# Optimization experiments

Measured on AMD Instinct MI355X. Metric: run time of the kernel, lower is better.

## Reference

```python
import jax, jax.numpy as jnp
import numpy as np

K_DIM = 1024
V_DIM = 1024
N_HEADS = 16
LN_EPS = 1e-5


def setup_inputs() -> dict:
    key = jax.random.key(0)
    ks = jax.random.split(key, 5)
    B, S = 16, 4096
    K = jax.random.normal(ks[0], (B, S, K_DIM), jnp.float32)
    V = jax.random.normal(ks[1], (B, S, V_DIM), jnp.float32)
    q = jax.random.normal(ks[2], (K_DIM,), jnp.float32)  # learned query
    w0_w = jax.random.normal(ks[3], (V_DIM, V_DIM), jnp.float32) / np.sqrt(V_DIM)
    w0_b = jnp.zeros((V_DIM,), jnp.float32)
    ln_g = jnp.ones((V_DIM,), jnp.float32)
    ln_b = jnp.zeros((V_DIM,), jnp.float32)
    return {"K": K, "V": V, "q": q, "w0_w": w0_w, "w0_b": w0_b, "ln_g": ln_g, "ln_b": ln_b}


def reference(K, V, q, w0_w, w0_b, ln_g, ln_b):
    B, S, C = K.shape
    H = N_HEADS
    d = C // H
    dv = V.shape[-1] // H
    # norm_query=True
    Q = q / jnp.linalg.norm(q)
    # expand to [B,1,C] then faithful contiguous view -> [B*H,1,d]
    Qh = jnp.broadcast_to(Q, (B, 1, C)).reshape(B * H, 1, d)
    # NOTE: the original uses a plain .view (row-major reshape), NOT a
    # transpose-based head split; we reproduce it exactly.
    Kh = K.reshape(B * H, S, d)
    Vh = V.reshape(B * H, S, dv)
    # torchtext ScaledDotProduct: softmax(Q K^T / sqrt(d)) V
    scale = 1.0 / jnp.sqrt(jnp.asarray(d, K.dtype))
    scores = jnp.einsum("bqd,bkd->bqk", Qh * scale, Kh)  # [B*H,1,S]
    attn = jax.nn.softmax(scores, axis=-1)
    A = jnp.einsum("bqk,bkd->bqd", attn, Vh)  # [B*H,1,dv]
    A = A.reshape(B, 1, H * dv)  # multihead_unshape
    # w0 linear
    A = A @ w0_w.T + w0_b
    # LayerNorm over last dim
    mu = jnp.mean(A, axis=-1, keepdims=True)
    var = jnp.var(A, axis=-1, keepdims=True)
    return ln_g * (A - mu) / jnp.sqrt(var + LN_EPS) + ln_b
```

## Files before the change

### kernel.cpp

```cpp
#include <hip/hip_runtime.h>

#define S_LEN 4096
#define D_HEAD 64
#define NH 16
#define C_DIM 1024
#define B_SZ 16
#define NG 256
#define ATTN_THREADS 512
#define NROWG (ATTN_THREADS / 16)

__global__ __launch_bounds__(ATTN_THREADS) void attn_kernel(
    const float* __restrict__ K, const float* __restrict__ V,
    const float* __restrict__ q, float* __restrict__ A)
{
    const int g   = blockIdx.x;
    const int h   = g & (NH - 1);
    const int tid = threadIdx.x;
    const int sub = tid & 15;
    const int rg  = tid >> 4;

    __shared__ float sc[S_LEN];
    __shared__ float part[NROWG * D_HEAD];
    __shared__ float red[ATTN_THREADS / 64];
    __shared__ float s_scalar;
    __shared__ __align__(16) float s_qs[D_HEAD];

    float p;
    {
        float a0 = q[tid];
        float a1 = q[tid + ATTN_THREADS];
        p = a0 * a0 + a1 * a1;
    }
    #pragma unroll
    for (int off = 32; off; off >>= 1) p += __shfl_xor(p, off);
    if ((tid & 63) == 0) red[tid >> 6] = p;
    __syncthreads();
    if (tid == 0) {
        float t = 0.f;
        #pragma unroll
        for (int w = 0; w < ATTN_THREADS / 64; w++) t += red[w];
        s_scalar = rsqrtf(t) * 0.125f;
    }
    __syncthreads();
    if (tid < D_HEAD) s_qs[tid] = q[h * D_HEAD + tid] * s_scalar;
    __syncthreads();

    const float4 qv = ((const float4*)s_qs)[sub];
    const float* __restrict__ Kg = K + (size_t)g * (S_LEN * D_HEAD);
    const float* __restrict__ Vg = V + (size_t)g * (S_LEN * D_HEAD);

    #pragma unroll 4
    for (int r = rg; r < S_LEN; r += NROWG) {
        float4 kv = ((const float4*)(Kg + r * D_HEAD))[sub];
        float d = kv.x * qv.x + kv.y * qv.y + kv.z * qv.z + kv.w * qv.w;
        d += __shfl_xor(d, 1);
        d += __shfl_xor(d, 2);
        d += __shfl_xor(d, 4);
        d += __shfl_xor(d, 8);
        if (sub == 0) sc[r] = d;
    }
    __syncthreads();

    float m = -3.4e38f;
    for (int i = tid; i < S_LEN; i += ATTN_THREADS) m = fmaxf(m, sc[i]);
    #pragma unroll
    for (int off = 32; off; off >>= 1) m = fmaxf(m, __shfl_xor(m, off));
    if ((tid & 63) == 0) red[tid >> 6] = m;
    __syncthreads();
    m = red[0];
    #pragma unroll
    for (int w = 1; w < ATTN_THREADS / 64; w++) m = fmaxf(m, red[w]);
    __syncthreads();

    float sum = 0.f;
    for (int i = tid; i < S_LEN; i += ATTN_THREADS) {
        float e = __expf(sc[i] - m);
        sc[i] = e;
        sum += e;
    }
    #pragma unroll
    for (int off = 32; off; off >>= 1) sum += __shfl_xor(sum, off);
    if ((tid & 63) == 0) red[tid >> 6] = sum;
    __syncthreads();
    float denom = 0.f;
    #pragma unroll
    for (int w = 0; w < ATTN_THREADS / 64; w++) denom += red[w];
    const float inv_denom = 1.0f / denom;

    float4 acc = make_float4(0.f, 0.f, 0.f, 0.f);
    #pragma unroll 4
    for (int r = rg; r < S_LEN; r += NROWG) {
        float4 vv = ((const float4*)(Vg + r * D_HEAD))[sub];
        float pr = sc[r];
        acc.x += pr * vv.x;
        acc.y += pr * vv.y;
        acc.z += pr * vv.z;
        acc.w += pr * vv.w;
    }
    ((float4*)part)[rg * 16 + sub] = acc;
    __syncthreads();
    if (tid < D_HEAD) {
        float s = 0.f;
        #pragma unroll
        for (int r2 = 0; r2 < NROWG; r2++) s += part[r2 * D_HEAD + tid];
        A[g * D_HEAD + tid] = s * inv_denom;
    }
}

__global__ __launch_bounds__(256) void proj_kernel(
    const float* __restrict__ A, const float* __restrict__ W,
    const float* __restrict__ bias, float* __restrict__ Y)
{
    const int j = blockIdx.x;
    const int tid = threadIdx.x;
    const float* __restrict__ Wj = W + (size_t)j * C_DIM;

    float acc[B_SZ];
    #pragma unroll
    for (int b = 0; b < B_SZ; b++) acc[b] = 0.f;

    for (int c = tid; c < C_DIM; c += 256) {
        float w = Wj[c];
        #pragma unroll
        for (int b = 0; b < B_SZ; b++) acc[b] += A[b * C_DIM + c] * w;
    }

    __shared__ float redw[B_SZ][4];
    #pragma unroll
    for (int b = 0; b < B_SZ; b++) {
        float v = acc[b];
        #pragma unroll
        for (int off = 32; off; off >>= 1) v += __shfl_xor(v, off);
        if ((tid & 63) == 0) redw[b][tid >> 6] = v;
    }
    __syncthreads();
    if (tid < B_SZ) {
        float s = redw[tid][0] + redw[tid][1] + redw[tid][2] + redw[tid][3];
        Y[tid * C_DIM + j] = s + bias[j];
    }
}

__global__ __launch_bounds__(256) void ln_kernel(
    const float* __restrict__ Y, const float* __restrict__ gam,
    const float* __restrict__ bet, float* __restrict__ out)
{
    const int b = blockIdx.x;
    const int tid = threadIdx.x;
    const float* __restrict__ Yb = Y + b * C_DIM;

    float vals[4];
    float s = 0.f, s2 = 0.f;
    #pragma unroll
    for (int i = 0; i < 4; i++) {
        float v = Yb[tid + i * 256];
        vals[i] = v;
        s += v;
        s2 += v * v;
    }
    #pragma unroll
    for (int off = 32; off; off >>= 1) {
        s  += __shfl_xor(s, off);
        s2 += __shfl_xor(s2, off);
    }
    __shared__ float rs[4], rs2[4];
    if ((tid & 63) == 0) { rs[tid >> 6] = s; rs2[tid >> 6] = s2; }
    __syncthreads();
    s  = rs[0] + rs[1] + rs[2] + rs[3];
    s2 = rs2[0] + rs2[1] + rs2[2] + rs2[3];
    const float mu  = s * (1.0f / C_DIM);
    const float var = s2 * (1.0f / C_DIM) - mu * mu;
    const float inv = rsqrtf(var + 1e-5f);
    #pragma unroll
    for (int i = 0; i < 4; i++) {
        int j = tid + i * 256;
        out[b * C_DIM + j] = gam[j] * (vals[i] - mu) * inv + bet[j];
    }
}

extern "C" void kernel_launch(void* const* d_in, const int* in_sizes, int n_in,
                              void* d_out, int out_size, void* d_ws, size_t ws_size,
                              hipStream_t stream) {
    const float* K    = (const float*)d_in[0];
    const float* V    = (const float*)d_in[1];
    const float* q    = (const float*)d_in[2];
    const float* w0_w = (const float*)d_in[3];
    const float* w0_b = (const float*)d_in[4];
    const float* ln_g = (const float*)d_in[5];
    const float* ln_b = (const float*)d_in[6];

    float* A = (float*)d_ws;
    float* Y = A + B_SZ * C_DIM;

    attn_kernel<<<NG, ATTN_THREADS, 0, stream>>>(K, V, q, A);
    proj_kernel<<<C_DIM, 256, 0, stream>>>(A, w0_w, w0_b, Y);
    ln_kernel<<<B_SZ, 256, 0, stream>>>(Y, ln_g, ln_b, (float*)d_out);
}
```

Measured before the change: 532.9 us.

## Split attention over sequence chunks with partial softmax and combine kernel

Attention is split into 8 sequence chunks per head group, giving 2048 blocks instead of 256. Each block computes a local max, a local sum and an unnormalized weighted V sum, and a separate combine kernel merges the chunks with rescaling. Query normalization moves into a tiny kernel of its own. The aim is to put more blocks in flight and raise memory parallelism on the bandwidth-bound K/V reads, at the price of extra launches and workspace traffic.

```diff
diff --git a/kernel.cpp b/kernel.cpp
--- a/kernel.cpp
+++ b/kernel.cpp
@@ -6,51 +6,58 @@
 #define C_DIM 1024
 #define B_SZ 16
 #define NG 256
-#define ATTN_THREADS 512
-#define NROWG (ATTN_THREADS / 16)
-
-__global__ __launch_bounds__(ATTN_THREADS) void attn_kernel(
+#define NSPLIT 8
+#define CHUNK (S_LEN / NSPLIT)
+#define TPB 256
+#define RG 16
+#define ITERS (CHUNK / RG)
+
+__global__ __launch_bounds__(256) void qnorm_kernel(
+    const float* __restrict__ q, float* __restrict__ qs)
+{
+    const int tid = threadIdx.x;
+    float v[4];
+    float p = 0.f;
+    #pragma unroll
+    for (int i = 0; i < 4; i++) {
+        v[i] = q[tid + i * 256];
+        p += v[i] * v[i];
+    }
+    #pragma unroll
+    for (int off = 32; off; off >>= 1) p += __shfl_xor(p, off);
+    __shared__ float red[4];
+    if ((tid & 63) == 0) red[tid >> 6] = p;
+    __syncthreads();
+    const float total = red[0] + red[1] + red[2] + red[3];
+    const float s = rsqrtf(total) * 0.125f;
+    #pragma unroll
+    for (int i = 0; i < 4; i++) qs[tid + i * 256] = v[i] * s;
+}
+
+__global__ __launch_bounds__(TPB) void attn_partial(
     const float* __restrict__ K, const float* __restrict__ V,
-    const float* __restrict__ q, float* __restrict__ A)
-{
-    const int g   = blockIdx.x;
-    const int h   = g & (NH - 1);
-    const int tid = threadIdx.x;
-    const int sub = tid & 15;
-    const int rg  = tid >> 4;
-
-    __shared__ float sc[S_LEN];
-    __shared__ float part[NROWG * D_HEAD];
-    __shared__ float red[ATTN_THREADS / 64];
-    __shared__ float s_scalar;
-    __shared__ __align__(16) float s_qs[D_HEAD];
-
-    float p;
-    {
-        float a0 = q[tid];
-        float a1 = q[tid + ATTN_THREADS];
-        p = a0 * a0 + a1 * a1;
-    }
-    #pragma unroll
-    for (int off = 32; off; off >>= 1) p += __shfl_xor(p, off);
-    if ((tid & 63) == 0) red[tid >> 6] = p;
-    __syncthreads();
-    if (tid == 0) {
-        float t = 0.f;
-        #pragma unroll
-        for (int w = 0; w < ATTN_THREADS / 64; w++) t += red[w];
-        s_scalar = rsqrtf(t) * 0.125f;
-    }
-    __syncthreads();
-    if (tid < D_HEAD) s_qs[tid] = q[h * D_HEAD + tid] * s_scalar;
-    __syncthreads();
-
-    const float4 qv = ((const float4*)s_qs)[sub];
-    const float* __restrict__ Kg = K + (size_t)g * (S_LEN * D_HEAD);
-    const float* __restrict__ Vg = V + (size_t)g * (S_LEN * D_HEAD);
-
-    #pragma unroll 4
-    for (int r = rg; r < S_LEN; r += NROWG) {
+    const float* __restrict__ qs, float* __restrict__ Apart,
+    float* __restrict__ mArr, float* __restrict__ lArr)
+{
+    const int blk   = blockIdx.x;
+    const int g     = blk >> 3;
+    const int split = blk & 7;
+    const int h     = g & (NH - 1);
+    const int tid   = threadIdx.x;
+    const int sub   = tid & 15;
+    const int rg    = tid >> 4;
+
+    __shared__ float sc[CHUNK];
+    __shared__ __align__(16) float part[RG * D_HEAD];
+    __shared__ float red[TPB / 64];
+
+    const float4 qv = ((const float4*)(qs + h * D_HEAD))[sub];
+    const float* __restrict__ Kg = K + ((size_t)g * S_LEN + (size_t)split * CHUNK) * D_HEAD;
+    const float* __restrict__ Vg = V + ((size_t)g * S_LEN + (size_t)split * CHUNK) * D_HEAD;
+
+    #pragma unroll 8
+    for (int i = 0; i < ITERS; i++) {
+        const int r = rg + i * RG;
         float4 kv = ((const float4*)(Kg + r * D_HEAD))[sub];
         float d = kv.x * qv.x + kv.y * qv.y + kv.z * qv.z + kv.w * qv.w;
         d += __shfl_xor(d, 1);
@@ -61,37 +68,31 @@
     }
     __syncthreads();
 
-    float m = -3.4e38f;
-    for (int i = tid; i < S_LEN; i += ATTN_THREADS) m = fmaxf(m, sc[i]);
+    float m = fmaxf(sc[tid], sc[tid + 256]);
     #pragma unroll
     for (int off = 32; off; off >>= 1) m = fmaxf(m, __shfl_xor(m, off));
     if ((tid & 63) == 0) red[tid >> 6] = m;
     __syncthreads();
-    m = red[0];
-    #pragma unroll
-    for (int w = 1; w < ATTN_THREADS / 64; w++) m = fmaxf(m, red[w]);
-    __syncthreads();
-
-    float sum = 0.f;
-    for (int i = tid; i < S_LEN; i += ATTN_THREADS) {
-        float e = __expf(sc[i] - m);
-        sc[i] = e;
-        sum += e;
-    }
+    m = fmaxf(fmaxf(red[0], red[1]), fmaxf(red[2], red[3]));
+    __syncthreads();
+
+    const float e0 = __expf(sc[tid] - m);
+    const float e1 = __expf(sc[tid + 256] - m);
+    sc[tid] = e0;
+    sc[tid + 256] = e1;
+    float sum = e0 + e1;
     #pragma unroll
     for (int off = 32; off; off >>= 1) sum += __shfl_xor(sum, off);
     if ((tid & 63) == 0) red[tid >> 6] = sum;
     __syncthreads();
-    float denom = 0.f;
-    #pragma unroll
-    for (int w = 0; w < ATTN_THREADS / 64; w++) denom += red[w];
-    const float inv_denom = 1.0f / denom;
+    const float lsum = red[0] + red[1] + red[2] + red[3];
 
     float4 acc = make_float4(0.f, 0.f, 0.f, 0.f);
-    #pragma unroll 4
-    for (int r = rg; r < S_LEN; r += NROWG) {
+    #pragma unroll 8
+    for (int i = 0; i < ITERS; i++) {
+        const int r = rg + i * RG;
         float4 vv = ((const float4*)(Vg + r * D_HEAD))[sub];
-        float pr = sc[r];
+        const float pr = sc[r];
         acc.x += pr * vv.x;
         acc.y += pr * vv.y;
         acc.z += pr * vv.z;
@@ -102,9 +103,36 @@
     if (tid < D_HEAD) {
         float s = 0.f;
         #pragma unroll
-        for (int r2 = 0; r2 < NROWG; r2++) s += part[r2 * D_HEAD + tid];
-        A[g * D_HEAD + tid] = s * inv_denom;
-    }
+        for (int r2 = 0; r2 < RG; r2++) s += part[r2 * D_HEAD + tid];
+        Apart[(size_t)blk * D_HEAD + tid] = s;
+    }
+    if (tid == 0) {
+        mArr[blk] = m;
+        lArr[blk] = lsum;
+    }
+}
+
+__global__ __launch_bounds__(64) void attn_combine(
+    const float* __restrict__ Apart, const float* __restrict__ mArr,
+    const float* __restrict__ lArr, float* __restrict__ A)
+{
+    const int g = blockIdx.x;
+    const int d = threadIdx.x;
+    float mv[NSPLIT];
+    float M = -3.4e38f;
+    #pragma unroll
+    for (int s = 0; s < NSPLIT; s++) {
+        mv[s] = mArr[g * NSPLIT + s];
+        M = fmaxf(M, mv[s]);
+    }
+    float denom = 0.f, acc = 0.f;
+    #pragma unroll
+    for (int s = 0; s < NSPLIT; s++) {
+        const float f = __expf(mv[s] - M);
+        denom += f * lArr[g * NSPLIT + s];
+        acc   += f * Apart[(size_t)(g * NSPLIT + s) * D_HEAD + d];
+    }
+    A[g * D_HEAD + d] = acc / denom;
 }
 
 __global__ __launch_bounds__(256) void proj_kernel(
@@ -119,8 +147,10 @@
     #pragma unroll
     for (int b = 0; b < B_SZ; b++) acc[b] = 0.f;
 
-    for (int c = tid; c < C_DIM; c += 256) {
-        float w = Wj[c];
+    #pragma unroll
+    for (int k = 0; k < 4; k++) {
+        const int c = tid + k * 256;
+        const float w = Wj[c];
         #pragma unroll
         for (int b = 0; b < B_SZ; b++) acc[b] += A[b * C_DIM + c] * w;
     }
@@ -135,7 +165,7 @@
     }
     __syncthreads();
     if (tid < B_SZ) {
-        float s = redw[tid][0] + redw[tid][1] + redw[tid][2] + redw[tid][3];
+        const float s = redw[tid][0] + redw[tid][1] + redw[tid][2] + redw[tid][3];
         Y[tid * C_DIM + j] = s + bias[j];
     }
 }
@@ -152,7 +182,7 @@
     float s = 0.f, s2 = 0.f;
     #pragma unroll
     for (int i = 0; i < 4; i++) {
-        float v = Yb[tid + i * 256];
+        const float v = Yb[tid + i * 256];
         vals[i] = v;
         s += v;
         s2 += v * v;
@@ -172,7 +202,7 @@
     const float inv = rsqrtf(var + 1e-5f);
     #pragma unroll
     for (int i = 0; i < 4; i++) {
-        int j = tid + i * 256;
+        const int j = tid + i * 256;
         out[b * C_DIM + j] = gam[j] * (vals[i] - mu) * inv + bet[j];
     }
 }
@@ -188,10 +218,16 @@
     const float* ln_g = (const float*)d_in[5];
     const float* ln_b = (const float*)d_in[6];
 
-    float* A = (float*)d_ws;
-    float* Y = A + B_SZ * C_DIM;
-
-    attn_kernel<<<NG, ATTN_THREADS, 0, stream>>>(K, V, q, A);
+    float* qs    = (float*)d_ws;
+    float* Apart = qs + C_DIM;
+    float* mArr  = Apart + (size_t)NG * NSPLIT * D_HEAD;
+    float* lArr  = mArr + NG * NSPLIT;
+    float* A     = lArr + NG * NSPLIT;
+    float* Y     = A + B_SZ * C_DIM;
+
+    qnorm_kernel<<<1, 256, 0, stream>>>(q, qs);
+    attn_partial<<<NG * NSPLIT, TPB, 0, stream>>>(K, V, qs, Apart, mArr, lArr);
+    attn_combine<<<NG, 64, 0, stream>>>(Apart, mArr, lArr, A);
     proj_kernel<<<C_DIM, 256, 0, stream>>>(A, w0_w, w0_b, Y);
     ln_kernel<<<B_SZ, 256, 0, stream>>>(Y, ln_g, ln_b, (float*)d_out);
 }
```

Result: no change. 524.3 us (-1.6%).
